# Kernel optimization log

Hardware: AMD Instinct MI355X
Metric: run time of the kernel (lower is better)

## Reference

```python
import jax, jax.numpy as jnp
import numpy as np

UNITS = 65536  # shape[0] * shape[1]
S0, S1 = 256, 256
BOND = 32
IN_DIM = 2     # forced by the original code's reshape([vec, vec], (2, 2))
BATCH = 2048


def setup_inputs() -> dict:
    key = jax.random.key(0)
    k_in, k_c1, k_c2 = jax.random.split(key, 3)
    inputs = jax.random.normal(k_in, (BATCH, IN_DIM), dtype=jnp.float32)
    # core_1: (input_dim, shape[0], bond), core_2: (input_dim, shape[1], bond)
    core1 = jax.random.normal(k_c1, (IN_DIM, S0, BOND), dtype=jnp.float32) * 0.05
    core2 = jax.random.normal(k_c2, (IN_DIM, S1, BOND), dtype=jnp.float32) * 0.05
    bias = jnp.zeros((S0, S1), dtype=jnp.float32)
    return {"inputs": inputs, "core1": core1, "core2": core2, "bias": bias}


def reference(inputs, core1, core2, bias):
    # Original per-sample op: x = reshape([vec, vec], (2,2)) so x[i, j] = vec[j];
    # ncon: result[a, c] = sum_{i,j,p} x[i,j] * core1[i,a,p] * core2[j,c,p]
    # Batched over all samples in one einsum (replaces tf.vectorized_map + ncon).
    X = jnp.stack([inputs, inputs], axis=1)            # (B, 2, 2), rows identical
    res = jnp.einsum('bij,iap,jcp->bac', X, core1, core2)  # (B, S0, S1)
    res = res + bias                                    # broadcast bias (S0, S1)
    return jax.nn.relu(res.reshape(-1, UNITS))          # (B, units)
```

## Files before the change

### kernel.cpp

```cpp
#include <hip/hip_runtime.h>

#define S0d   256
#define S1d   256
#define BONDd 32
#define BATCHd 2048
#define UNITSd 65536

typedef float f32x4 __attribute__((ext_vector_type(4)));
typedef float f32x2 __attribute__((ext_vector_type(2)));

__global__ __launch_bounds__(256) void precompute_G(
    const float* __restrict__ core1, const float* __restrict__ core2,
    float* __restrict__ G) {
  const int u = blockIdx.x * 256 + threadIdx.x;
  const int a = u >> 8;
  const int c = u & 255;
  const f32x4* c10 = (const f32x4*)(core1 + a * BONDd);
  const f32x4* c11 = (const f32x4*)(core1 + S0d * BONDd + a * BONDd);
  const f32x4* r0  = (const f32x4*)(core2 + c * BONDd);
  const f32x4* r1  = (const f32x4*)(core2 + S1d * BONDd + c * BONDd);
  float acc0 = 0.f, acc1 = 0.f;
#pragma unroll
  for (int q = 0; q < BONDd / 4; ++q) {
    f32x4 x = c10[q], y = c11[q];
    f32x4 s = x + y;
    f32x4 v0 = r0[q], v1 = r1[q];
    acc0 = fmaf(s.x, v0.x, fmaf(s.y, v0.y, fmaf(s.z, v0.z, fmaf(s.w, v0.w, acc0))));
    acc1 = fmaf(s.x, v1.x, fmaf(s.y, v1.y, fmaf(s.z, v1.z, fmaf(s.w, v1.w, acc1))));
  }
  G[u] = acc0;
  G[UNITSd + u] = acc1;
}

__global__ __launch_bounds__(256) void td_row(
    const float* __restrict__ inputs, const float* __restrict__ G,
    const float* __restrict__ bias, float* __restrict__ out) {
  const int b = blockIdx.x;
  const f32x2 x = *(const f32x2*)(inputs + b * 2);
  float* outp = out + (size_t)b * UNITSd;
  const int base = threadIdx.x * 4;
#pragma unroll 4
  for (int it = 0; it < UNITSd / 1024; ++it) {
    const int u = it * 1024 + base;
    const f32x4 g0 = *(const f32x4*)(G + u);
    const f32x4 g1 = *(const f32x4*)(G + UNITSd + u);
    const f32x4 bs = *(const f32x4*)(bias + u);
    f32x4 r;
    r.x = fmaxf(fmaf(x.y, g1.x, fmaf(x.x, g0.x, bs.x)), 0.f);
    r.y = fmaxf(fmaf(x.y, g1.y, fmaf(x.x, g0.y, bs.y)), 0.f);
    r.z = fmaxf(fmaf(x.y, g1.z, fmaf(x.x, g0.z, bs.z)), 0.f);
    r.w = fmaxf(fmaf(x.y, g1.w, fmaf(x.x, g0.w, bs.w)), 0.f);
    __builtin_nontemporal_store(r, (f32x4*)(outp + u));
  }
}

__global__ __launch_bounds__(256) void td_fused(
    const float* __restrict__ inputs, const float* __restrict__ core1,
    const float* __restrict__ core2, const float* __restrict__ bias,
    float* __restrict__ out) {
  const int u = blockIdx.x * 1024 + threadIdx.x * 4;
  const int a = u >> 8;
  const int c = u & 255;
  float s[BONDd];
#pragma unroll
  for (int p = 0; p < BONDd; ++p)
    s[p] = core1[a * BONDd + p] + core1[S0d * BONDd + a * BONDd + p];
  float g0[4], g1[4];
#pragma unroll
  for (int cc = 0; cc < 4; ++cc) {
    float a0 = 0.f, a1 = 0.f;
#pragma unroll
    for (int p = 0; p < BONDd; ++p) {
      a0 = fmaf(s[p], core2[(c + cc) * BONDd + p], a0);
      a1 = fmaf(s[p], core2[S1d * BONDd + (c + cc) * BONDd + p], a1);
    }
    g0[cc] = a0; g1[cc] = a1;
  }
  const f32x4 bs = *(const f32x4*)(bias + u);
  const int b0 = blockIdx.y * 64;
  float* outp = out + (size_t)b0 * UNITSd + u;
#pragma unroll 4
  for (int k = 0; k < 64; ++k) {
    const f32x2 x = *(const f32x2*)(inputs + (b0 + k) * 2);
    f32x4 r;
    r.x = fmaxf(fmaf(x.y, g1[0], fmaf(x.x, g0[0], bs.x)), 0.f);
    r.y = fmaxf(fmaf(x.y, g1[1], fmaf(x.x, g0[1], bs.y)), 0.f);
    r.z = fmaxf(fmaf(x.y, g1[2], fmaf(x.x, g0[2], bs.z)), 0.f);
    r.w = fmaxf(fmaf(x.y, g1[3], fmaf(x.x, g0[3], bs.w)), 0.f);
    *(f32x4*)outp = r;
    outp += UNITSd;
  }
}

extern "C" void kernel_launch(void* const* d_in, const int* in_sizes, int n_in,
                              void* d_out, int out_size, void* d_ws, size_t ws_size,
                              hipStream_t stream) {
  const float* inputs = (const float*)d_in[0];
  const float* core1  = (const float*)d_in[1];
  const float* core2  = (const float*)d_in[2];
  const float* bias   = (const float*)d_in[3];
  float* out = (float*)d_out;

  const size_t g_bytes = (size_t)2 * UNITSd * sizeof(float);
  if (ws_size >= g_bytes) {
    float* G = (float*)d_ws;
    precompute_G<<<UNITSd / 256, 256, 0, stream>>>(core1, core2, G);
    td_row<<<BATCHd, 256, 0, stream>>>(inputs, G, bias, out);
  } else {
    td_fused<<<dim3(UNITSd / 1024, BATCHd / 64), 256, 0, stream>>>(
        inputs, core1, core2, bias, out);
  }
}
```

Measured before the change: 111.1 us.

## Tile output kernel over units and batch to reuse G and bias in registers

Replaces the per-row kernel with a 2D tiled kernel where each block owns a 4096-unit chunk across 32 batch rows. G and bias values are loaded into registers once per block and reused for every row, so far fewer reads of G and bias are issued than when every sample re-read them. The output write traffic stays the same, so the gain is limited by store bandwidth, and the store pattern now strides by a full row between iterations.

```diff
diff --git a/kernel.cpp b/kernel.cpp
--- a/kernel.cpp
+++ b/kernel.cpp
@@ -5,6 +5,8 @@
 #define BONDd 32
 #define BATCHd 2048
 #define UNITSd 65536
+#define UCH   4096
+#define NB    32
 
 typedef float f32x4 __attribute__((ext_vector_type(4)));
 typedef float f32x2 __attribute__((ext_vector_type(2)));
@@ -32,25 +34,32 @@
   G[UNITSd + u] = acc1;
 }
 
-__global__ __launch_bounds__(256) void td_row(
+__global__ __launch_bounds__(256) void td_tile(
     const float* __restrict__ inputs, const float* __restrict__ G,
     const float* __restrict__ bias, float* __restrict__ out) {
-  const int b = blockIdx.x;
-  const f32x2 x = *(const f32x2*)(inputs + b * 2);
-  float* outp = out + (size_t)b * UNITSd;
-  const int base = threadIdx.x * 4;
-#pragma unroll 4
-  for (int it = 0; it < UNITSd / 1024; ++it) {
-    const int u = it * 1024 + base;
-    const f32x4 g0 = *(const f32x4*)(G + u);
-    const f32x4 g1 = *(const f32x4*)(G + UNITSd + u);
-    const f32x4 bs = *(const f32x4*)(bias + u);
-    f32x4 r;
-    r.x = fmaxf(fmaf(x.y, g1.x, fmaf(x.x, g0.x, bs.x)), 0.f);
-    r.y = fmaxf(fmaf(x.y, g1.y, fmaf(x.x, g0.y, bs.y)), 0.f);
-    r.z = fmaxf(fmaf(x.y, g1.z, fmaf(x.x, g0.z, bs.z)), 0.f);
-    r.w = fmaxf(fmaf(x.y, g1.w, fmaf(x.x, g0.w, bs.w)), 0.f);
-    __builtin_nontemporal_store(r, (f32x4*)(outp + u));
+  const int u0 = blockIdx.x * UCH + threadIdx.x * 4;
+  f32x4 g0[4], g1[4], bs[4];
+#pragma unroll
+  for (int q = 0; q < 4; ++q) {
+    const int u = u0 + q * 1024;
+    g0[q] = *(const f32x4*)(G + u);
+    g1[q] = *(const f32x4*)(G + UNITSd + u);
+    bs[q] = *(const f32x4*)(bias + u);
+  }
+  const int b0 = blockIdx.y * NB;
+  float* outp = out + (size_t)b0 * UNITSd + u0;
+  for (int k = 0; k < NB; ++k) {
+    const f32x2 x = *(const f32x2*)(inputs + (b0 + k) * 2);
+#pragma unroll
+    for (int q = 0; q < 4; ++q) {
+      f32x4 r;
+      r.x = fmaxf(fmaf(x.y, g1[q].x, fmaf(x.x, g0[q].x, bs[q].x)), 0.f);
+      r.y = fmaxf(fmaf(x.y, g1[q].y, fmaf(x.x, g0[q].y, bs[q].y)), 0.f);
+      r.z = fmaxf(fmaf(x.y, g1[q].z, fmaf(x.x, g0[q].z, bs[q].z)), 0.f);
+      r.w = fmaxf(fmaf(x.y, g1[q].w, fmaf(x.x, g0[q].w, bs[q].w)), 0.f);
+      __builtin_nontemporal_store(r, (f32x4*)(outp + q * 1024));
+    }
+    outp += UNITSd;
   }
 }
 
@@ -105,7 +114,8 @@
   if (ws_size >= g_bytes) {
     float* G = (float*)d_ws;
     precompute_G<<<UNITSd / 256, 256, 0, stream>>>(core1, core2, G);
-    td_row<<<BATCHd, 256, 0, stream>>>(inputs, G, bias, out);
+    td_tile<<<dim3(UNITSd / UCH, BATCHd / NB), 256, 0, stream>>>(
+        inputs, G, bias, out);
   } else {
     td_fused<<<dim3(UNITSd / 1024, BATCHd / 64), 256, 0, stream>>>(
         inputs, core1, core2, bias, out);
```

Result: slower. 119.3 us (+7.4%).

## Store precomputed G and bias as packed bf16 and stream per-wave with prefetch

Applied to the files above, without the earlier changes.

The precompute kernel now computes four adjacent outputs per thread, reusing the summed core1 row, and stores both G planes and the bias as packed bf16 pairs in an interleaved record. The row kernel reads these half-size records, gives each wave a contiguous chunk, and software-prefetches the next record. The aim is to cut the bytes read per output element, although the 512 MB fp32 output write still dominates traffic. Rounding G and bias to bf16 loses precision and may fail a tight tolerance.

```diff
diff --git a/kernel.cpp b/kernel.cpp
--- a/kernel.cpp
+++ b/kernel.cpp
@@ -5,52 +5,90 @@
 #define BONDd 32
 #define BATCHd 2048
 #define UNITSd 65536
+#define NQ    16384
 
 typedef float f32x4 __attribute__((ext_vector_type(4)));
 typedef float f32x2 __attribute__((ext_vector_type(2)));
+typedef unsigned int u32;
+typedef u32 u32x4 __attribute__((ext_vector_type(4)));
+typedef u32 u32x2 __attribute__((ext_vector_type(2)));
 
-__global__ __launch_bounds__(256) void precompute_G(
+__device__ __forceinline__ u32 f2bf(float f) {
+  u32 u = __float_as_uint(f);
+  return (u + 0x7fffu + ((u >> 16) & 1u)) >> 16;
+}
+__device__ __forceinline__ float bf_lo(u32 w) { return __uint_as_float(w << 16); }
+__device__ __forceinline__ float bf_hi(u32 w) { return __uint_as_float(w & 0xffff0000u); }
+
+__global__ __launch_bounds__(256) void precompute_GB(
     const float* __restrict__ core1, const float* __restrict__ core2,
-    float* __restrict__ G) {
-  const int u = blockIdx.x * 256 + threadIdx.x;
-  const int a = u >> 8;
-  const int c = u & 255;
+    const float* __restrict__ bias, u32x4* __restrict__ GB, u32x2* __restrict__ Bb) {
+  const int q = blockIdx.x * 256 + threadIdx.x;
+  const int a = q >> 6;
+  const int c0 = (q & 63) * 4;
+  f32x4 sv[BONDd / 4];
   const f32x4* c10 = (const f32x4*)(core1 + a * BONDd);
   const f32x4* c11 = (const f32x4*)(core1 + S0d * BONDd + a * BONDd);
-  const f32x4* r0  = (const f32x4*)(core2 + c * BONDd);
-  const f32x4* r1  = (const f32x4*)(core2 + S1d * BONDd + c * BONDd);
-  float acc0 = 0.f, acc1 = 0.f;
 #pragma unroll
-  for (int q = 0; q < BONDd / 4; ++q) {
-    f32x4 x = c10[q], y = c11[q];
-    f32x4 s = x + y;
-    f32x4 v0 = r0[q], v1 = r1[q];
-    acc0 = fmaf(s.x, v0.x, fmaf(s.y, v0.y, fmaf(s.z, v0.z, fmaf(s.w, v0.w, acc0))));
-    acc1 = fmaf(s.x, v1.x, fmaf(s.y, v1.y, fmaf(s.z, v1.z, fmaf(s.w, v1.w, acc1))));
+  for (int qq = 0; qq < BONDd / 4; ++qq) sv[qq] = c10[qq] + c11[qq];
+  float g0[4], g1[4];
+#pragma unroll
+  for (int e = 0; e < 4; ++e) {
+    const f32x4* r0 = (const f32x4*)(core2 + (c0 + e) * BONDd);
+    const f32x4* r1 = (const f32x4*)(core2 + S1d * BONDd + (c0 + e) * BONDd);
+    float a0 = 0.f, a1 = 0.f;
+#pragma unroll
+    for (int qq = 0; qq < BONDd / 4; ++qq) {
+      f32x4 s = sv[qq], v0 = r0[qq], v1 = r1[qq];
+      a0 = fmaf(s.x, v0.x, fmaf(s.y, v0.y, fmaf(s.z, v0.z, fmaf(s.w, v0.w, a0))));
+      a1 = fmaf(s.x, v1.x, fmaf(s.y, v1.y, fmaf(s.z, v1.z, fmaf(s.w, v1.w, a1))));
+    }
+    g0[e] = a0; g1[e] = a1;
   }
-  G[u] = acc0;
-  G[UNITSd + u] = acc1;
+  u32x4 gb;
+  gb.x = f2bf(g0[0]) | (f2bf(g0[1]) << 16);
+  gb.y = f2bf(g0[2]) | (f2bf(g0[3]) << 16);
+  gb.z = f2bf(g1[0]) | (f2bf(g1[1]) << 16);
+  gb.w = f2bf(g1[2]) | (f2bf(g1[3]) << 16);
+  GB[q] = gb;
+  const f32x4 bs = *(const f32x4*)(bias + q * 4);
+  u32x2 bb;
+  bb.x = f2bf(bs.x) | (f2bf(bs.y) << 16);
+  bb.y = f2bf(bs.z) | (f2bf(bs.w) << 16);
+  Bb[q] = bb;
 }
 
-__global__ __launch_bounds__(256) void td_row(
-    const float* __restrict__ inputs, const float* __restrict__ G,
-    const float* __restrict__ bias, float* __restrict__ out) {
+__global__ __launch_bounds__(256) void td_wave_bf(
+    const float* __restrict__ inputs, const u32x4* __restrict__ GB,
+    const u32x2* __restrict__ Bb, float* __restrict__ out) {
   const int b = blockIdx.x;
   const f32x2 x = *(const f32x2*)(inputs + b * 2);
-  float* outp = out + (size_t)b * UNITSd;
-  const int base = threadIdx.x * 4;
+  const int wave = threadIdx.x >> 6;
+  const int lane = threadIdx.x & 63;
+  const int q0 = wave * (NQ / 4) + lane;
+  f32x4* outv = (f32x4*)(out + (size_t)b * UNITSd) + q0;
+
+  u32x4 gbn = GB[q0];
+  u32x2 bbn = Bb[q0];
 #pragma unroll 4
-  for (int it = 0; it < UNITSd / 1024; ++it) {
-    const int u = it * 1024 + base;
-    const f32x4 g0 = *(const f32x4*)(G + u);
-    const f32x4 g1 = *(const f32x4*)(G + UNITSd + u);
-    const f32x4 bs = *(const f32x4*)(bias + u);
+  for (int it = 0; it < 63; ++it) {
+    const u32x4 gb = gbn; const u32x2 bb = bbn;
+    gbn = GB[q0 + (it + 1) * 64];
+    bbn = Bb[q0 + (it + 1) * 64];
     f32x4 r;
-    r.x = fmaxf(fmaf(x.y, g1.x, fmaf(x.x, g0.x, bs.x)), 0.f);
-    r.y = fmaxf(fmaf(x.y, g1.y, fmaf(x.x, g0.y, bs.y)), 0.f);
-    r.z = fmaxf(fmaf(x.y, g1.z, fmaf(x.x, g0.z, bs.z)), 0.f);
-    r.w = fmaxf(fmaf(x.y, g1.w, fmaf(x.x, g0.w, bs.w)), 0.f);
-    __builtin_nontemporal_store(r, (f32x4*)(outp + u));
+    r.x = fmaxf(fmaf(x.y, bf_lo(gb.z), fmaf(x.x, bf_lo(gb.x), bf_lo(bb.x))), 0.f);
+    r.y = fmaxf(fmaf(x.y, bf_hi(gb.z), fmaf(x.x, bf_hi(gb.x), bf_hi(bb.x))), 0.f);
+    r.z = fmaxf(fmaf(x.y, bf_lo(gb.w), fmaf(x.x, bf_lo(gb.y), bf_lo(bb.y))), 0.f);
+    r.w = fmaxf(fmaf(x.y, bf_hi(gb.w), fmaf(x.x, bf_hi(gb.y), bf_hi(bb.y))), 0.f);
+    __builtin_nontemporal_store(r, outv + it * 64);
+  }
+  {
+    f32x4 r;
+    r.x = fmaxf(fmaf(x.y, bf_lo(gbn.z), fmaf(x.x, bf_lo(gbn.x), bf_lo(bbn.x))), 0.f);
+    r.y = fmaxf(fmaf(x.y, bf_hi(gbn.z), fmaf(x.x, bf_hi(gbn.x), bf_hi(bbn.x))), 0.f);
+    r.z = fmaxf(fmaf(x.y, bf_lo(gbn.w), fmaf(x.x, bf_lo(gbn.y), bf_lo(bbn.y))), 0.f);
+    r.w = fmaxf(fmaf(x.y, bf_hi(gbn.w), fmaf(x.x, bf_hi(gbn.y), bf_hi(bbn.y))), 0.f);
+    __builtin_nontemporal_store(r, outv + 63 * 64);
   }
 }
 
@@ -101,11 +139,12 @@
   const float* bias   = (const float*)d_in[3];
   float* out = (float*)d_out;
 
-  const size_t g_bytes = (size_t)2 * UNITSd * sizeof(float);
-  if (ws_size >= g_bytes) {
-    float* G = (float*)d_ws;
-    precompute_G<<<UNITSd / 256, 256, 0, stream>>>(core1, core2, G);
-    td_row<<<BATCHd, 256, 0, stream>>>(inputs, G, bias, out);
+  const size_t need = (size_t)NQ * 16 + (size_t)NQ * 8;
+  if (ws_size >= need) {
+    u32x4* GB = (u32x4*)d_ws;
+    u32x2* Bb = (u32x2*)((char*)d_ws + (size_t)NQ * 16);
+    precompute_GB<<<NQ / 256, 256, 0, stream>>>(core1, core2, bias, GB, Bb);
+    td_wave_bf<<<BATCHd, 256, 0, stream>>>(inputs, GB, Bb, out);
   } else {
     td_fused<<<dim3(UNITSd / 1024, BATCHd / 64), 256, 0, stream>>>(
         inputs, core1, core2, bias, out);
```

After: 113.7 us. 2.3% more time.
